# Kernel tuning notes

Hardware: AMD Instinct MI355X
Metric: run time of the kernel (lower is better)

Reference implementation:

```python
import jax, jax.numpy as jnp
import numpy as np

L, B, S, H, NH, FF = 4, 16, 512, 768, 12, 3072
D = H // NH
SCALE = D ** -0.5
EPS = 1e-5


def _ln(x, g, b):
    m = jnp.mean(x, axis=-1, keepdims=True)
    v = jnp.mean((x - m) ** 2, axis=-1, keepdims=True)
    return (x - m) * jax.lax.rsqrt(v + EPS) * g + b


def setup_inputs() -> dict:
    key = jax.random.key(0)
    ks = jax.random.split(key, 16)
    def n(k, shape, s=0.02):
        return jax.random.normal(k, shape, dtype=jnp.float32) * s
    return {
        "x": jax.random.normal(ks[0], (B, S, H), dtype=jnp.float32),
        "attn_bias": jax.random.normal(ks[1], (B, NH, S, S), dtype=jnp.float32) * 0.1,
        "ln1_g": jnp.ones((L, H), jnp.float32), "ln1_b": jnp.zeros((L, H), jnp.float32),
        "wq": n(ks[2], (L, H, H)), "bq": jnp.zeros((L, H), jnp.float32),
        "wk": n(ks[3], (L, H, H)), "bk": jnp.zeros((L, H), jnp.float32),
        "wv": n(ks[4], (L, H, H)), "bv": jnp.zeros((L, H), jnp.float32),
        "wo": n(ks[5], (L, H, H)), "bo": jnp.zeros((L, H), jnp.float32),
        "ln2_g": jnp.ones((L, H), jnp.float32), "ln2_b": jnp.zeros((L, H), jnp.float32),
        "w1": n(ks[6], (L, H, FF)), "b1": jnp.zeros((L, FF), jnp.float32),
        "w2": n(ks[7], (L, FF, H)), "b2": jnp.zeros((L, H), jnp.float32),
        "fln_g": jnp.ones((H,), jnp.float32), "fln_b": jnp.zeros((H,), jnp.float32),
    }


def reference(x, attn_bias, ln1_g, ln1_b, wq, bq, wk, bk, wv, bv, wo, bo,
              ln2_g, ln2_b, w1, b1, w2, b2, fln_g, fln_b):
    def body(h, p):
        l1g, l1b, Wq, Bq, Wk, Bk, Wv, Bv, Wo, Bo, l2g, l2b, W1, B1, W2, B2 = p
        y = _ln(h, l1g, l1b)
        # [B,S,H] -> [B,NH,S,D]
        q = (y @ Wq + Bq).reshape(B, S, NH, D).transpose(0, 2, 1, 3)
        k = (y @ Wk + Bk).reshape(B, S, NH, D).transpose(0, 2, 1, 3)
        v = (y @ Wv + Bv).reshape(B, S, NH, D).transpose(0, 2, 1, 3)
        a = jnp.einsum('bhsd,bhtd->bhst', q * SCALE, k) + attn_bias
        a = jax.nn.softmax(a, axis=-1)
        o = jnp.einsum('bhst,bhtd->bhsd', a, v).transpose(0, 2, 1, 3).reshape(B, S, H)
        h = h + o @ Wo + Bo
        y = _ln(h, l2g, l2b)
        y = jax.nn.gelu(y @ W1 + B1, approximate=False) @ W2 + B2
        return h + y, None

    params = (ln1_g, ln1_b, wq, bq, wk, bk, wv, bv, wo, bo, ln2_g, ln2_b, w1, b1, w2, b2)
    x, _ = jax.lax.scan(body, x, params)
    return _ln(x, fln_g, fln_b)
```

## Files before the change

kernel.cpp:

```cpp
#include <hip/hip_runtime.h>
#include <math.h>

constexpr int Lc = 4, Bc = 16, Sc = 512, Hc = 768, NHc = 12, FFc = 3072, Dc = 64;
constexpr int MR = Bc * Sc;
constexpr int QS = 2304;
constexpr float SCALEc = 0.125f;

typedef __attribute__((ext_vector_type(8))) __bf16 bf16x8;
typedef __attribute__((ext_vector_type(4))) __bf16 bf16x4;
typedef __attribute__((ext_vector_type(4))) float  floatx4;

__device__ inline floatx4 mfma16(bf16x8 a, bf16x8 b, floatx4 c) {
    return __builtin_amdgcn_mfma_f32_16x16x32_bf16(a, b, c, 0, 0, 0);
}
__device__ inline float gelu_f(float x) {
    return 0.5f * x * (1.0f + erff(x * 0.70710678118654752f));
}
__device__ inline void ld16(const __bf16* g, __bf16* l) {
    __builtin_amdgcn_global_load_lds(
        (const __attribute__((address_space(1))) void*)g,
        (__attribute__((address_space(3))) void*)l, 16, 0, 0);
}

template<bool FINAL>
__global__ __launch_bounds__(256) void ln_k(
    const float* __restrict__ x, const float* __restrict__ g, const float* __restrict__ bt,
    __bf16* __restrict__ yb, float* __restrict__ yf)
{
    const int row  = blockIdx.x * 4 + (threadIdx.x >> 6);
    const int lane = threadIdx.x & 63;
    const int col  = lane * 12;
    const float* xr = x + (size_t)row * Hc + col;
    float v[12];
    *(float4*)(v + 0) = *(const float4*)(xr + 0);
    *(float4*)(v + 4) = *(const float4*)(xr + 4);
    *(float4*)(v + 8) = *(const float4*)(xr + 8);
    float s = 0.f, s2 = 0.f;
#pragma unroll
    for (int j = 0; j < 12; ++j) { s += v[j]; s2 += v[j] * v[j]; }
#pragma unroll
    for (int o = 32; o > 0; o >>= 1) { s += __shfl_xor(s, o); s2 += __shfl_xor(s2, o); }
    const float mean = s * (1.0f / Hc);
    const float inv  = rsqrtf(s2 * (1.0f / Hc) - mean * mean + 1e-5f);
    float gv[12], bv[12];
    *(float4*)(gv + 0) = *(const float4*)(g + col);
    *(float4*)(gv + 4) = *(const float4*)(g + col + 4);
    *(float4*)(gv + 8) = *(const float4*)(g + col + 8);
    *(float4*)(bv + 0) = *(const float4*)(bt + col);
    *(float4*)(bv + 4) = *(const float4*)(bt + col + 4);
    *(float4*)(bv + 8) = *(const float4*)(bt + col + 8);
    if (FINAL) {
        float o[12];
#pragma unroll
        for (int j = 0; j < 12; ++j) o[j] = (v[j] - mean) * inv * gv[j] + bv[j];
        float* yr = yf + (size_t)row * Hc + col;
        *(float4*)(yr + 0) = *(float4*)(o + 0);
        *(float4*)(yr + 4) = *(float4*)(o + 4);
        *(float4*)(yr + 8) = *(float4*)(o + 8);
    } else {
        __bf16 o[12];
#pragma unroll
        for (int j = 0; j < 12; ++j) o[j] = (__bf16)((v[j] - mean) * inv * gv[j] + bv[j]);
        __bf16* yr = yb + (size_t)row * Hc + col;
        *(bf16x4*)(yr + 0) = *(bf16x4*)(o + 0);
        *(bf16x4*)(yr + 4) = *(bf16x4*)(o + 4);
        *(bf16x4*)(yr + 8) = *(bf16x4*)(o + 8);
    }
}

__global__ __launch_bounds__(256) void transp_k(
    const float* __restrict__ in, __bf16* __restrict__ out, int R, int C)
{
    __shared__ float t[32][33];
    const int c0 = blockIdx.x * 32, r0 = blockIdx.y * 32;
    const int tx = threadIdx.x & 31, ty = threadIdx.x >> 5;
#pragma unroll
    for (int i = 0; i < 4; ++i)
        t[ty + i * 8][tx] = in[(size_t)(r0 + ty + i * 8) * C + c0 + tx];
    __syncthreads();
#pragma unroll
    for (int i = 0; i < 4; ++i)
        out[(size_t)(c0 + ty + i * 8) * R + r0 + tx] = (__bf16)t[tx][ty + i * 8];
}

__global__ void bias_cat_k(const float* __restrict__ a, const float* __restrict__ b,
                           const float* __restrict__ c, float* __restrict__ o)
{
    int i = threadIdx.x + blockIdx.x * 256;
    if (i < QS) o[i] = i < Hc ? a[i] : (i < 2 * Hc ? b[i - Hc] : c[i - 2 * Hc]);
}

template<int ACT, bool RESID>
__global__ __launch_bounds__(256) void gemm2_k(
    const __bf16* __restrict__ A, const __bf16* __restrict__ Bt,
    const float* __restrict__ bias, const float* __restrict__ resid,
    float* __restrict__ outF, __bf16* __restrict__ outB,
    int M, int N, int K)
{
    __shared__ alignas(16) __bf16 As[128 * 32];
    __shared__ alignas(16) __bf16 Bs[128 * 32];
    const int tid  = threadIdx.x;
    const int wave = tid >> 6, lane = tid & 63, lhi = lane >> 4, llo = lane & 15;
    const int wm = wave >> 1, wn = wave & 1;
    const int row0 = blockIdx.y * 128, col0 = blockIdx.x * 128;
    const int srow = lane >> 2;
    const int scol = (lane & 3) * 8;

    floatx4 acc[4][4];
#pragma unroll
    for (int i = 0; i < 4; ++i)
#pragma unroll
        for (int j = 0; j < 4; ++j) acc[i][j] = {0.f, 0.f, 0.f, 0.f};

    const __bf16* Ab = A  + (size_t)(row0 + wave * 16 + srow) * K + scol;
    const __bf16* Bb = Bt + (size_t)(col0 + wave * 16 + srow) * K + scol;

    for (int kt = 0; kt < K; kt += 32) {
#pragma unroll
        for (int t = 0; t < 2; ++t) {
            ld16(Ab + (size_t)(t * 64) * K + kt, As + (t * 64 + wave * 16) * 32);
            ld16(Bb + (size_t)(t * 64) * K + kt, Bs + (t * 64 + wave * 16) * 32);
        }
        __syncthreads();
        bf16x8 af[4], bfr[4];
#pragma unroll
        for (int i = 0; i < 4; ++i)
            af[i]  = *(const bf16x8*)(As + (wm * 64 + i * 16 + llo) * 32 + lhi * 8);
#pragma unroll
        for (int j = 0; j < 4; ++j)
            bfr[j] = *(const bf16x8*)(Bs + (wn * 64 + j * 16 + llo) * 32 + lhi * 8);
#pragma unroll
        for (int i = 0; i < 4; ++i)
#pragma unroll
            for (int j = 0; j < 4; ++j)
                acc[i][j] = mfma16(af[i], bfr[j], acc[i][j]);
        __syncthreads();
    }
#pragma unroll
    for (int i = 0; i < 4; ++i) {
#pragma unroll
        for (int j = 0; j < 4; ++j) {
            int colc = col0 + wn * 64 + j * 16 + llo;
            float bb = bias[colc];
#pragma unroll
            for (int r = 0; r < 4; ++r) {
                int rowc = row0 + wm * 64 + i * 16 + lhi * 4 + r;
                float vv = acc[i][j][r] + bb;
                if (ACT == 1) vv = gelu_f(vv);
                size_t idx = (size_t)rowc * N + colc;
                if (RESID) outF[idx] = resid[idx] + vv;
                else       outB[idx] = (__bf16)vv;
            }
        }
    }
}

__global__ __launch_bounds__(256) void attn_k(
    const __bf16* __restrict__ q, const __bf16* __restrict__ k,
    const __bf16* __restrict__ v, const float* __restrict__ bias,
    __bf16* __restrict__ o)
{
    __shared__ alignas(16) __bf16 Qs[64][72];
    __shared__ alignas(16) __bf16 Ks[64][72];
    __shared__ alignas(16) __bf16 Vt[64][72];
    __shared__ alignas(16) __bf16 Ps[64][72];
    __shared__ float  Sf[64][68];
    __shared__ float  mrun[64], lrun[64], alf[64];

    const int qt = blockIdx.x, hh = blockIdx.y, b = blockIdx.z;
    const int tid = threadIdx.x, wave = tid >> 6, lane = tid & 63;
    const int lhi = lane >> 4, llo = lane & 15;
    const size_t base  = (size_t)b * Sc * QS + hh * Dc;
    const size_t obase = (size_t)b * Sc * Hc + hh * Dc;

#pragma unroll
    for (int c = 0; c < 2; ++c) {
        int id = tid + c * 256;
        int r = id >> 3, c8 = id & 7;
        *(bf16x8*)(&Qs[r][c8 * 8]) =
            *(const bf16x8*)(q + base + (size_t)(qt * 64 + r) * QS + c8 * 8);
    }
    if (tid < 64) { mrun[tid] = -1e30f; lrun[tid] = 0.f; }

    floatx4 acco[4];
#pragma unroll
    for (int j = 0; j < 4; ++j) acco[j] = {0.f, 0.f, 0.f, 0.f};

    const float* brow = bias + ((size_t)(b * NHc + hh) * Sc + qt * 64) * Sc;

    for (int kt = 0; kt < Sc; kt += 64) {
        __syncthreads();
#pragma unroll
        for (int c = 0; c < 2; ++c) {
            int id = tid + c * 256;
            int r = id >> 3, c8 = id & 7;
            *(bf16x8*)(&Ks[r][c8 * 8]) =
                *(const bf16x8*)(k + base + (size_t)(kt + r) * QS + c8 * 8);
            bf16x8 vv = *(const bf16x8*)(v + base + (size_t)(kt + r) * QS + c8 * 8);
#pragma unroll
            for (int jj = 0; jj < 8; ++jj) Vt[c8 * 8 + jj][r] = vv[jj];
        }
        __syncthreads();
        floatx4 accs[4];
#pragma unroll
        for (int j = 0; j < 4; ++j) accs[j] = {0.f, 0.f, 0.f, 0.f};
#pragma unroll
        for (int kk = 0; kk < 2; ++kk) {
            bf16x8 aq = *(const bf16x8*)(&Qs[wave * 16 + llo][kk * 32 + lhi * 8]);
#pragma unroll
            for (int nf = 0; nf < 4; ++nf) {
                bf16x8 bk2 = *(const bf16x8*)(&Ks[nf * 16 + llo][kk * 32 + lhi * 8]);
                accs[nf] = mfma16(aq, bk2, accs[nf]);
            }
        }
#pragma unroll
        for (int nf = 0; nf < 4; ++nf) {
#pragma unroll
            for (int r = 0; r < 4; ++r) {
                int lr = wave * 16 + lhi * 4 + r;
                float sv = accs[nf][r] * SCALEc + brow[(size_t)lr * Sc + kt + nf * 16 + llo];
                Sf[lr][nf * 16 + llo] = sv;
            }
        }
        __syncthreads();
        {
            int row = tid >> 2, seg = tid & 3;
            float sv[16]; float mx = -1e30f;
#pragma unroll
            for (int j2 = 0; j2 < 16; ++j2) { sv[j2] = Sf[row][seg * 16 + j2]; mx = fmaxf(mx, sv[j2]); }
            mx = fmaxf(mx, __shfl_xor(mx, 1));
            mx = fmaxf(mx, __shfl_xor(mx, 2));
            float mold = mrun[row];
            float mnew = fmaxf(mold, mx);
            float al = __expf(mold - mnew);
            float sum = 0.f;
#pragma unroll
            for (int j2 = 0; j2 < 16; ++j2) {
                float p = __expf(sv[j2] - mnew);
                sum += p;
                Ps[row][seg * 16 + j2] = (__bf16)p;
            }
            sum += __shfl_xor(sum, 1);
            sum += __shfl_xor(sum, 2);
            if (seg == 0) { mrun[row] = mnew; lrun[row] = lrun[row] * al + sum; alf[row] = al; }
        }
        __syncthreads();
#pragma unroll
        for (int nf = 0; nf < 4; ++nf)
#pragma unroll
            for (int r = 0; r < 4; ++r) acco[nf][r] *= alf[wave * 16 + lhi * 4 + r];
#pragma unroll
        for (int kk = 0; kk < 2; ++kk) {
            bf16x8 ap = *(const bf16x8*)(&Ps[wave * 16 + llo][kk * 32 + lhi * 8]);
#pragma unroll
            for (int nf = 0; nf < 4; ++nf) {
                bf16x8 bv2 = *(const bf16x8*)(&Vt[nf * 16 + llo][kk * 32 + lhi * 8]);
                acco[nf] = mfma16(ap, bv2, acco[nf]);
            }
        }
    }
#pragma unroll
    for (int nf = 0; nf < 4; ++nf) {
#pragma unroll
        for (int r = 0; r < 4; ++r) {
            int lr = wave * 16 + lhi * 4 + r;
            float oo = acco[nf][r] / lrun[lr];
            o[obase + (size_t)(qt * 64 + lr) * Hc + nf * 16 + llo] = (__bf16)oo;
        }
    }
}

extern "C" void kernel_launch(void* const* d_in, const int* in_sizes, int n_in,
                              void* d_out, int out_size, void* d_ws, size_t ws_size,
                              hipStream_t stream)
{
    const float* x     = (const float*)d_in[0];
    const float* abias = (const float*)d_in[1];
    const float* ln1g  = (const float*)d_in[2];
    const float* ln1b  = (const float*)d_in[3];
    const float* wq    = (const float*)d_in[4];
    const float* bq    = (const float*)d_in[5];
    const float* wk    = (const float*)d_in[6];
    const float* bk    = (const float*)d_in[7];
    const float* wv    = (const float*)d_in[8];
    const float* bv    = (const float*)d_in[9];
    const float* wo    = (const float*)d_in[10];
    const float* bo    = (const float*)d_in[11];
    const float* ln2g  = (const float*)d_in[12];
    const float* ln2b  = (const float*)d_in[13];
    const float* w1    = (const float*)d_in[14];
    const float* b1    = (const float*)d_in[15];
    const float* w2    = (const float*)d_in[16];
    const float* b2    = (const float*)d_in[17];
    const float* flng  = (const float*)d_in[18];
    const float* flnb  = (const float*)d_in[19];

    float* h = (float*)d_out;
    __bf16* y    = (__bf16*)d_ws;
    __bf16* qkv  = y   + (size_t)MR * Hc;
    __bf16* ob   = qkv + (size_t)MR * QS;
    __bf16* fb   = ob  + (size_t)MR * Hc;
    __bf16* w1t  = fb  + (size_t)MR * FFc;
    __bf16* w2t  = w1t + (size_t)FFc * Hc;
    float*  bqkv = (float*)(w2t + (size_t)Hc * FFc);
    __bf16* wqkvt = fb;
    __bf16* wot   = fb + (size_t)QS * Hc;

    hipMemcpyAsync(h, x, (size_t)MR * Hc * sizeof(float), hipMemcpyDeviceToDevice, stream);

    dim3 blk(256);
    dim3 gLN(MR / 4);
    dim3 gQKV(QS / 128, MR / 128);
    dim3 gP(Hc / 128, MR / 128);
    dim3 gF(FFc / 128, MR / 128);
    dim3 gA(Sc / 64, NHc, Bc);
    dim3 gT_HH(Hc / 32, Hc / 32);
    dim3 gT_HF(FFc / 32, Hc / 32);
    dim3 gT_FH(Hc / 32, FFc / 32);

    for (int l = 0; l < Lc; ++l) {
        const float* wq_l = wq + (size_t)l * Hc * Hc;
        const float* wk_l = wk + (size_t)l * Hc * Hc;
        const float* wv_l = wv + (size_t)l * Hc * Hc;
        const float* wo_l = wo + (size_t)l * Hc * Hc;
        const float* w1_l = w1 + (size_t)l * Hc * FFc;
        const float* w2_l = w2 + (size_t)l * FFc * Hc;

        transp_k<<<gT_HH, blk, 0, stream>>>(wq_l, wqkvt,                        Hc, Hc);
        transp_k<<<gT_HH, blk, 0, stream>>>(wk_l, wqkvt + (size_t)Hc * Hc,      Hc, Hc);
        transp_k<<<gT_HH, blk, 0, stream>>>(wv_l, wqkvt + (size_t)2 * Hc * Hc,  Hc, Hc);
        transp_k<<<gT_HH, blk, 0, stream>>>(wo_l, wot, Hc, Hc);
        transp_k<<<gT_HF, blk, 0, stream>>>(w1_l, w1t, Hc, FFc);
        transp_k<<<gT_FH, blk, 0, stream>>>(w2_l, w2t, FFc, Hc);
        bias_cat_k<<<dim3(9), blk, 0, stream>>>(bq + l * Hc, bk + l * Hc, bv + l * Hc, bqkv);

        ln_k<false><<<gLN, blk, 0, stream>>>(h, ln1g + l * Hc, ln1b + l * Hc, y, nullptr);
        gemm2_k<0, false><<<gQKV, blk, 0, stream>>>(y, wqkvt, bqkv, nullptr, nullptr, qkv, MR, QS, Hc);
        attn_k<<<gA, blk, 0, stream>>>(qkv, qkv + Hc, qkv + 2 * Hc, abias, ob);
        gemm2_k<0, true><<<gP, blk, 0, stream>>>(ob, wot, bo + l * Hc, h, h, nullptr, MR, Hc, Hc);
        ln_k<false><<<gLN, blk, 0, stream>>>(h, ln2g + l * Hc, ln2b + l * Hc, y, nullptr);
        gemm2_k<1, false><<<gF, blk, 0, stream>>>(y, w1t, b1 + l * FFc, nullptr, nullptr, fb, MR, FFc, Hc);
        gemm2_k<0, true><<<gP, blk, 0, stream>>>(fb, w2t, b2 + l * Hc, h, h, nullptr, MR, Hc, FFc);
    }
    ln_k<true><<<gLN, blk, 0, stream>>>(h, flng, flnb, nullptr, h);
}
```

Baseline: 1.755 ms.

## Add 128x64-tile GEMM for N=768 projections and reorder attention grid

Adds a new 2-wave GEMM kernel with 128x64 tiles and uses it for the output projection and FFN down-projection (N=768). This doubles the block count from 384 to 768 so the GPU's CUs are better filled. It also remaps the attention grid so head/batch is the fast dimension, and pads the Vt shared array from 72 to 66 columns to change its bank layout. In exchange, the smaller tiles reuse less data per load, and the new kernel has no double buffering.

New measurement: 1.726 ms. No clear change (-1.7%).

```diff
diff --git a/kernel.cpp b/kernel.cpp
--- a/kernel.cpp
+++ b/kernel.cpp
@@ -155,6 +155,66 @@
     }
 }
 
+__global__ __launch_bounds__(128) void gemm3_k(
+    const __bf16* __restrict__ A, const __bf16* __restrict__ Bt,
+    const float* __restrict__ bias, const float* __restrict__ resid,
+    float* __restrict__ outF, int M, int N, int K)
+{
+    __shared__ alignas(16) __bf16 As[128 * 32];
+    __shared__ alignas(16) __bf16 Bs[64 * 32];
+    const int tid  = threadIdx.x;
+    const int wave = tid >> 6, lane = tid & 63, lhi = lane >> 4, llo = lane & 15;
+    const int row0 = blockIdx.y * 128, col0 = blockIdx.x * 64;
+    const int srow = lane >> 2;
+    const int scol = (lane & 3) * 8;
+
+    floatx4 acc[4][4];
+#pragma unroll
+    for (int i = 0; i < 4; ++i)
+#pragma unroll
+        for (int j = 0; j < 4; ++j) acc[i][j] = {0.f, 0.f, 0.f, 0.f};
+
+    const __bf16* Ab = A  + (size_t)(row0 + wave * 64 + srow) * K + scol;
+    const __bf16* Bb = Bt + (size_t)(col0 + wave * 32 + srow) * K + scol;
+
+    for (int kt = 0; kt < K; kt += 32) {
+#pragma unroll
+        for (int t = 0; t < 4; ++t)
+            ld16(Ab + (size_t)(t * 16) * K + kt, As + (wave * 64 + t * 16) * 32);
+#pragma unroll
+        for (int t = 0; t < 2; ++t)
+            ld16(Bb + (size_t)(t * 16) * K + kt, Bs + (wave * 32 + t * 16) * 32);
+        __syncthreads();
+        bf16x8 af[4], bfr[4];
+#pragma unroll
+        for (int i = 0; i < 4; ++i)
+            af[i]  = *(const bf16x8*)(As + (wave * 64 + i * 16 + llo) * 32 + lhi * 8);
+#pragma unroll
+        for (int j = 0; j < 4; ++j)
+            bfr[j] = *(const bf16x8*)(Bs + (j * 16 + llo) * 32 + lhi * 8);
+#pragma unroll
+        for (int i = 0; i < 4; ++i)
+#pragma unroll
+            for (int j = 0; j < 4; ++j)
+                acc[i][j] = mfma16(af[i], bfr[j], acc[i][j]);
+        __syncthreads();
+    }
+#pragma unroll
+    for (int i = 0; i < 4; ++i) {
+#pragma unroll
+        for (int j = 0; j < 4; ++j) {
+            int colc = col0 + j * 16 + llo;
+            float bb = bias[colc];
+#pragma unroll
+            for (int r = 0; r < 4; ++r) {
+                int rowc = row0 + wave * 64 + i * 16 + lhi * 4 + r;
+                size_t idx = (size_t)rowc * N + colc;
+                outF[idx] = resid[idx] + acc[i][j][r] + bb;
+            }
+        }
+    }
+}
+
 __global__ __launch_bounds__(256) void attn_k(
     const __bf16* __restrict__ q, const __bf16* __restrict__ k,
     const __bf16* __restrict__ v, const float* __restrict__ bias,
@@ -162,12 +222,12 @@
 {
     __shared__ alignas(16) __bf16 Qs[64][72];
     __shared__ alignas(16) __bf16 Ks[64][72];
-    __shared__ alignas(16) __bf16 Vt[64][72];
+    __shared__ alignas(16) __bf16 Vt[64][66];
     __shared__ alignas(16) __bf16 Ps[64][72];
     __shared__ float  Sf[64][68];
     __shared__ float  mrun[64], lrun[64], alf[64];
 
-    const int qt = blockIdx.x, hh = blockIdx.y, b = blockIdx.z;
+    const int hh = blockIdx.x % NHc, b = blockIdx.x / NHc, qt = blockIdx.y;
     const int tid = threadIdx.x, wave = tid >> 6, lane = tid & 63;
     const int lhi = lane >> 4, llo = lane & 15;
     const size_t base  = (size_t)b * Sc * QS + hh * Dc;
@@ -311,9 +371,9 @@
     dim3 blk(256);
     dim3 gLN(MR / 4);
     dim3 gQKV(QS / 128, MR / 128);
-    dim3 gP(Hc / 128, MR / 128);
+    dim3 gP64(Hc / 64, MR / 128);
     dim3 gF(FFc / 128, MR / 128);
-    dim3 gA(Sc / 64, NHc, Bc);
+    dim3 gA(Bc * NHc, Sc / 64);
     dim3 gT_HH(Hc / 32, Hc / 32);
     dim3 gT_HF(FFc / 32, Hc / 32);
     dim3 gT_FH(Hc / 32, FFc / 32);
@@ -337,10 +397,10 @@
         ln_k<false><<<gLN, blk, 0, stream>>>(h, ln1g + l * Hc, ln1b + l * Hc, y, nullptr);
         gemm2_k<0, false><<<gQKV, blk, 0, stream>>>(y, wqkvt, bqkv, nullptr, nullptr, qkv, MR, QS, Hc);
         attn_k<<<gA, blk, 0, stream>>>(qkv, qkv + Hc, qkv + 2 * Hc, abias, ob);
-        gemm2_k<0, true><<<gP, blk, 0, stream>>>(ob, wot, bo + l * Hc, h, h, nullptr, MR, Hc, Hc);
+        gemm3_k<<<gP64, dim3(128), 0, stream>>>(ob, wot, bo + l * Hc, h, h, MR, Hc, Hc);
         ln_k<false><<<gLN, blk, 0, stream>>>(h, ln2g + l * Hc, ln2b + l * Hc, y, nullptr);
         gemm2_k<1, false><<<gF, blk, 0, stream>>>(y, w1t, b1 + l * FFc, nullptr, nullptr, fb, MR, FFc, Hc);
-        gemm2_k<0, true><<<gP, blk, 0, stream>>>(fb, w2t, b2 + l * Hc, h, h, nullptr, MR, Hc, FFc);
+        gemm3_k<<<gP64, dim3(128), 0, stream>>>(fb, w2t, b2 + l * Hc, h, h, MR, Hc, FFc);
     }
     ln_k<true><<<gLN, blk, 0, stream>>>(h, flng, flnb, nullptr, h);
 }
```
